# Kernel optimization log

Measured on AMD Instinct MI355X. Metric: run time of the kernel, lower is better.

Reference implementation:

```python
import jax, jax.numpy as jnp
import numpy as np

DIM = 128
N_NODES = 100000
N_EDGES = 600000
LN_EPS = 1e-5


def setup_inputs() -> dict:
    key = jax.random.key(0)
    k_x, k_ei, k_ew, k_w, k_b, k_g = jax.random.split(key, 6)
    x = jax.random.normal(k_x, (N_NODES, DIM), dtype=jnp.float32)
    edge_index = jax.random.randint(k_ei, (2, N_EDGES), 0, N_NODES, dtype=jnp.int64)
    edge_weight = jax.random.uniform(k_ew, (N_EDGES,), dtype=jnp.float32, minval=0.05, maxval=1.0)
    # GCNConv linear weight (glorot) + bias; LayerNorm affine params
    limit = float(np.sqrt(6.0 / (DIM + DIM)))
    W = jax.random.uniform(k_w, (DIM, DIM), dtype=jnp.float32, minval=-limit, maxval=limit)
    b = jnp.zeros((DIM,), dtype=jnp.float32)
    gamma = jnp.ones((DIM,), dtype=jnp.float32)
    beta = jnp.zeros((DIM,), dtype=jnp.float32)
    return {"x": x, "edge_index": edge_index, "edge_weight": edge_weight,
            "W": W, "b": b, "gamma": gamma, "beta": beta}


def reference(x, edge_index, edge_weight, W, b, gamma, beta):
    N = x.shape[0]
    row, col = edge_index[0], edge_index[1]  # messages flow row -> col (source_to_target)

    # gcn_norm (add_self_loops=False): deg[j] = sum of incoming edge weights
    deg = jax.ops.segment_sum(edge_weight, col, num_segments=N)
    deg_safe = jnp.where(deg > 0, deg, 1.0)
    dinv = jnp.where(deg > 0, jax.lax.rsqrt(deg_safe), 0.0)
    norm = dinv[row] * edge_weight * dinv[col]  # [E]

    h = x @ W                                   # [N, D] linear transform
    msg = h[row] * norm[:, None]                # gather + scale [E, D]
    agg = jax.ops.segment_sum(msg, col, num_segments=N) + b  # scatter-add [N, D]

    # LayerNorm over feature dim
    mu = jnp.mean(agg, axis=-1, keepdims=True)
    var = jnp.mean((agg - mu) ** 2, axis=-1, keepdims=True)
    ln = (agg - mu) * jax.lax.rsqrt(var + LN_EPS) * gamma + beta

    # GELU (torch default = exact erf form); dropout is identity at eval
    return x + jax.nn.gelu(ln, approximate=False)
```

## Files before the change

kernel.cpp:

```cpp
#include <hip/hip_runtime.h>
#include <hip/hip_fp16.h>
#include <math.h>

#define DIM 128
#define TR 32
#define SA_STRIDE 136
#define CSR_CAP 1024

#define DEG_SHIFT 42
#define DEG_SCALE 33554432.0f
#define DEG_MASK ((1ull << DEG_SHIFT) - 1)

typedef __attribute__((ext_vector_type(8))) short s16x8;
typedef __attribute__((ext_vector_type(4))) float f32x4;

__device__ __forceinline__ ushort f2bf(float f) {
    union { float f; unsigned u; } v; v.f = f;
    unsigned u = v.u;
    return (ushort)((u + 0x7FFFu + ((u >> 16) & 1u)) >> 16);
}

__device__ __forceinline__ ushort f2h(float f) {
    __half h = __float2half_rn(f);
    return *reinterpret_cast<ushort*>(&h);
}

__device__ __forceinline__ float h2f(ushort u) {
    __half_raw hr; hr.x = u;
    return __half2float(__half(hr));
}

__global__ void fill_zero(float* p, int n) {
    int i = blockIdx.x * blockDim.x + threadIdx.x;
    if (i < n) p[i] = 0.f;
}

__global__ void fill_zero4(float4* p, int n4) {
    int i = blockIdx.x * blockDim.x + threadIdx.x;
    if (i < n4) p[i] = make_float4(0.f, 0.f, 0.f, 0.f);
}

__global__ void init_kernel(const float* __restrict__ W, ushort* __restrict__ Wt,
                            float* __restrict__ zbase, int nz, int* __restrict__ gctr) {
    int i = blockIdx.x * blockDim.x + threadIdx.x;
    if (i < 16384) {
        int k = i >> 7, n = i & 127;
        Wt[n * DIM + k] = f2bf(W[k * DIM + n]);
    }
    int z = i - 16384;
    if (z >= 0 && z < nz) zbase[z] = 0.f;
    if (i == 0) *gctr = 0;
}

__global__ void count_deg_kernel(const int* __restrict__ ei, const float* __restrict__ ew,
                                 unsigned long long* __restrict__ cd,
                                 int* __restrict__ rank,
                                 const float* __restrict__ x, ushort* __restrict__ xh,
                                 int nxh, int E) {
    int e = blockIdx.x * blockDim.x + threadIdx.x;
    int nthreads = gridDim.x * blockDim.x;
    unsigned long long old = 0;
    bool valid = (e < E);
    if (valid) {
        int col = ei[E + e];
        unsigned long long pk = (1ull << DEG_SHIFT)
                              + (unsigned long long)(ew[e] * DEG_SCALE + 0.5f);
        old = atomicAdd(&cd[col], pk);
    }
    const float4* xs = (const float4*)x;
    for (int i = e; i < nxh; i += nthreads) {
        float4 a = xs[i * 2], c = xs[i * 2 + 1];
        s16x8 h;
        h[0] = (short)f2h(a.x); h[1] = (short)f2h(a.y);
        h[2] = (short)f2h(a.z); h[3] = (short)f2h(a.w);
        h[4] = (short)f2h(c.x); h[5] = (short)f2h(c.y);
        h[6] = (short)f2h(c.z); h[7] = (short)f2h(c.w);
        *(s16x8*)&xh[i * 8] = h;
    }
    if (valid) rank[e] = (int)(old >> DEG_SHIFT);
}

__global__ __launch_bounds__(256) void alloc_kernel(const unsigned long long* __restrict__ cd,
                                                    float* __restrict__ dinv,
                                                    int* __restrict__ row_start,
                                                    int* __restrict__ row_end,
                                                    int* __restrict__ gctr, int N) {
    __shared__ int wsum[4];
    __shared__ int sbase;
    int t = threadIdx.x;
    int i = blockIdx.x * 256 + t;
    int lane = t & 63;
    int w = t >> 6;
    unsigned long long p = (i < N) ? cd[i] : 0ull;
    int c = (int)(p >> DEG_SHIFT);
    int pre = c;
#pragma unroll
    for (int off = 1; off < 64; off <<= 1) {
        int v = __shfl_up(pre, off);
        if (lane >= off) pre += v;
    }
    if (lane == 63) wsum[w] = pre;
    __syncthreads();
    if (t == 0) sbase = atomicAdd(gctr, wsum[0] + wsum[1] + wsum[2] + wsum[3]);
    __syncthreads();
    int woff = 0;
#pragma unroll
    for (int k = 0; k < 3; ++k) if (w > k) woff += wsum[k];
    if (i < N) {
        int rs = sbase + woff + pre - c;
        row_start[i] = rs;
        row_end[i] = rs + c;
        float d = (float)(p & DEG_MASK) * (1.0f / DEG_SCALE);
        dinv[i] = d > 0.f ? rsqrtf(d) : 0.f;
    }
}

__global__ void csr_fill_kernel(const int* __restrict__ ei, const float* __restrict__ ew,
                                const int* __restrict__ rank,
                                const int* __restrict__ row_start,
                                const float* __restrict__ dinv,
                                int2* __restrict__ csr, int E) {
    int e = blockIdx.x * blockDim.x + threadIdx.x;
    if (e < E) {
        int row = ei[e];
        int col = ei[E + e];
        int p = row_start[col] + rank[e];
        float w = dinv[row] * ew[e];
        csr[p] = make_int2(row, __float_as_int(w));
    }
}

template<bool XH>
__global__ __launch_bounds__(256) void gather_mfma_ln_kernel(
        const int2* __restrict__ csr, const int* __restrict__ row_start,
        const int* __restrict__ seg_end, const float* __restrict__ dinv,
        const float* __restrict__ x, const ushort* __restrict__ xh,
        const ushort* __restrict__ Wt, const float* __restrict__ b,
        const float* __restrict__ gamma, const float* __restrict__ beta,
        float* __restrict__ out, int N) {
    __shared__ ushort sA[TR * SA_STRIDE];
    __shared__ int2 sCsr[CSR_CAP];
    __shared__ float redS[4][16];
    __shared__ float redQ[4][16];

    const int tid  = threadIdx.x;
    const int lane = tid & 63;
    const int w    = tid >> 6;
    const int row0 = blockIdx.x * TR;

    if (XH) {
        int lastNode = row0 + TR - 1; if (lastNode > N - 1) lastNode = N - 1;
        const int S = row_start[row0];
        const int T = seg_end[lastNode];
        const int M = T - S;
        const bool useLds = (M <= CSR_CAP);
        if (useLds) {
            for (int i = tid; i < M; i += 256) sCsr[i] = csr[S + i];
        }
        __syncthreads();

        const int l16 = tid & 15;
        const int g16 = tid >> 4;
        const s16x8* xh8 = (const s16x8*)xh;
        int sidx[2], eidx[2];
        float dv[2];
        float accq[2][8];
#pragma unroll
        for (int q = 0; q < 2; ++q) {
            int node = row0 + g16 * 2 + q;
            int ok = node < N;
            sidx[q] = ok ? row_start[node] : 0;
            eidx[q] = ok ? seg_end[node] : 0;
            dv[q]   = ok ? dinv[node] : 0.f;
#pragma unroll
            for (int e8 = 0; e8 < 8; ++e8) accq[q][e8] = 0.f;
        }

        if (useLds) {
#pragma unroll
            for (int q = 0; q < 2; ++q) {
                int sL = sidx[q] - S, eL = eidx[q] - S;
#pragma unroll 2
                for (int j = sL; j < eL; j += 2) {
                    int2 e0 = sCsr[j];
                    bool v1 = (j + 1) < eL;
                    int2 e1 = sCsr[v1 ? j + 1 : j];
                    float w0 = __int_as_float(e0.y);
                    float w1 = v1 ? __int_as_float(e1.y) : 0.f;
                    s16x8 r0 = xh8[(size_t)e0.x * 16 + l16];
                    s16x8 r1 = xh8[(size_t)e1.x * 16 + l16];
#pragma unroll
                    for (int e8 = 0; e8 < 8; ++e8) {
                        accq[q][e8] += w0 * h2f((ushort)r0[e8]);
                        accq[q][e8] += w1 * h2f((ushort)r1[e8]);
                    }
                }
            }
        } else {
            int maxlen = 0;
#pragma unroll
            for (int q = 0; q < 2; ++q) {
                int len = eidx[q] - sidx[q];
                maxlen = len > maxlen ? len : maxlen;
            }
#pragma unroll 2
            for (int it = 0; it < maxlen; ++it) {
                int2 pk[2];
#pragma unroll
                for (int q = 0; q < 2; ++q) {
                    int j = sidx[q] + it;
                    pk[q] = csr[j < eidx[q] ? j : 0];
                }
#pragma unroll
                for (int q = 0; q < 2; ++q) {
                    float wt = (sidx[q] + it < eidx[q]) ? __int_as_float(pk[q].y) : 0.f;
                    s16x8 hv = xh8[(size_t)pk[q].x * 16 + l16];
#pragma unroll
                    for (int e8 = 0; e8 < 8; ++e8)
                        accq[q][e8] += wt * h2f((ushort)hv[e8]);
                }
            }
        }
#pragma unroll
        for (int q = 0; q < 2; ++q) {
            int r = g16 * 2 + q;
            s16x8 p8;
#pragma unroll
            for (int e8 = 0; e8 < 8; ++e8) p8[e8] = (short)f2bf(accq[q][e8] * dv[q]);
            *(s16x8*)&sA[r * SA_STRIDE + l16 * 8] = p8;
        }
    } else {
        const int l32 = tid & 31;
        const int g32 = tid >> 5;
        const float4* xv = (const float4*)x;
        int sidx[4], eidx[4];
        float dv[4];
        float4 accq[4];
        int maxlen = 0;
#pragma unroll
        for (int q = 0; q < 4; ++q) {
            int node = row0 + g32 * 4 + q;
            int ok = node < N;
            sidx[q] = ok ? row_start[node] : 0;
            eidx[q] = ok ? seg_end[node] : 0;
            dv[q]   = ok ? dinv[node] : 0.f;
            accq[q] = make_float4(0.f, 0.f, 0.f, 0.f);
            int len = eidx[q] - sidx[q];
            maxlen = len > maxlen ? len : maxlen;
        }
#pragma unroll 2
        for (int it = 0; it < maxlen; ++it) {
            int2 pk[4];
#pragma unroll
            for (int q = 0; q < 4; ++q) {
                int j = sidx[q] + it;
                pk[q] = csr[j < eidx[q] ? j : 0];
            }
#pragma unroll
            for (int q = 0; q < 4; ++q) {
                float wt = (sidx[q] + it < eidx[q]) ? __int_as_float(pk[q].y) : 0.f;
                float4 v = xv[(size_t)pk[q].x * 32 + l32];
                accq[q].x += wt * v.x; accq[q].y += wt * v.y;
                accq[q].z += wt * v.z; accq[q].w += wt * v.w;
            }
        }
#pragma unroll
        for (int q = 0; q < 4; ++q) {
            int r = g32 * 4 + q;
            ushort4 p4;
            p4.x = f2bf(accq[q].x * dv[q]); p4.y = f2bf(accq[q].y * dv[q]);
            p4.z = f2bf(accq[q].z * dv[q]); p4.w = f2bf(accq[q].w * dv[q]);
            *(ushort4*)&sA[r * SA_STRIDE + l32 * 4] = p4;
        }
    }
    __syncthreads();

    const int m16  = lane & 15;
    const int quad = lane >> 4;
    const int tm   = w & 1;
    const int tnb  = (w >> 1) * 4;

    s16x8 afrag[4];
    const ushort* arow = &sA[(16 * tm + m16) * SA_STRIDE + quad * 8];
#pragma unroll
    for (int kb = 0; kb < 4; ++kb)
        afrag[kb] = *(const s16x8*)(arow + kb * 32);

    f32x4 acc[4];
#pragma unroll
    for (int t = 0; t < 4; ++t) { acc[t][0] = 0.f; acc[t][1] = 0.f; acc[t][2] = 0.f; acc[t][3] = 0.f; }

#pragma unroll
    for (int kb = 0; kb < 4; ++kb) {
#pragma unroll
        for (int t = 0; t < 4; ++t) {
            const ushort* bp = Wt + (size_t)((tnb + t) * 16 + m16) * DIM + kb * 32 + quad * 8;
            s16x8 bfrag = *(const s16x8*)bp;
            acc[t] = __builtin_amdgcn_mfma_f32_16x16x32_bf16(afrag[kb], bfrag, acc[t], 0, 0, 0);
        }
    }

    float gcol[4], becol[4];
#pragma unroll
    for (int t = 0; t < 4; ++t) {
        int col = (tnb + t) * 16 + m16;
        float bc = b[col];
        gcol[t]  = gamma[col];
        becol[t] = beta[col];
#pragma unroll
        for (int i = 0; i < 4; ++i) acc[t][i] += bc;
    }

    float s[4], sq[4];
#pragma unroll
    for (int i = 0; i < 4; ++i) {
        s[i]  = acc[0][i] + acc[1][i] + acc[2][i] + acc[3][i];
        sq[i] = acc[0][i]*acc[0][i] + acc[1][i]*acc[1][i] + acc[2][i]*acc[2][i] + acc[3][i]*acc[3][i];
    }
#pragma unroll
    for (int off = 1; off <= 8; off <<= 1) {
#pragma unroll
        for (int i = 0; i < 4; ++i) {
            s[i]  += __shfl_xor(s[i], off);
            sq[i] += __shfl_xor(sq[i], off);
        }
    }
    if (m16 == 0) {
#pragma unroll
        for (int i = 0; i < 4; ++i) {
            redS[w][quad * 4 + i] = s[i];
            redQ[w][quad * 4 + i] = sq[i];
        }
    }
    __syncthreads();

#pragma unroll
    for (int i = 0; i < 4; ++i) {
        int rloc = quad * 4 + i;
        float tot  = redS[w][rloc] + redS[w ^ 2][rloc];
        float totq = redQ[w][rloc] + redQ[w ^ 2][rloc];
        float mu   = tot * (1.0f / DIM);
        float var  = totq * (1.0f / DIM) - mu * mu;
        float rstd = rsqrtf(var + 1e-5f);
        int r = row0 + 16 * tm + rloc;
        if (r < N) {
#pragma unroll
            for (int t = 0; t < 4; ++t) {
                int col = (tnb + t) * 16 + m16;
                float l = (acc[t][i] - mu) * rstd * gcol[t] + becol[t];
                float g = 0.5f * l * (1.0f + erff(l * 0.70710678118654752f));
                out[(size_t)r * DIM + col] = x[(size_t)r * DIM + col] + g;
            }
        }
    }
}

__global__ void deg_kernel(const int* __restrict__ ei, const float* __restrict__ ew,
                           float* __restrict__ deg, int E) {
    int e = blockIdx.x * blockDim.x + threadIdx.x;
    if (e < E) atomicAdd(&deg[ei[E + e]], ew[e]);
}

__global__ void dinv_kernel(float* deg, int N) {
    int i = blockIdx.x * blockDim.x + threadIdx.x;
    if (i < N) {
        float d = deg[i];
        deg[i] = d > 0.f ? rsqrtf(d) : 0.f;
    }
}

__global__ void scatter_kernel(const int* __restrict__ ei, const float* __restrict__ ew,
                               const float* __restrict__ dinv, const float* __restrict__ x,
                               float* __restrict__ out, int E) {
    int t = blockIdx.x * blockDim.x + threadIdx.x;
    int e = t >> 5;
    if (e >= E) return;
    int lane = t & 31;
    int row = ei[e];
    int col = ei[E + e];
    float w = dinv[row] * ew[e] * dinv[col];
    float4 v = *(const float4*)(x + (size_t)row * DIM + (lane << 2));
    float* dst = out + (size_t)col * DIM + (lane << 2);
    atomicAdd(dst + 0, v.x * w);
    atomicAdd(dst + 1, v.y * w);
    atomicAdd(dst + 2, v.z * w);
    atomicAdd(dst + 3, v.w * w);
}

__global__ __launch_bounds__(256) void gemm_ln_kernel(const float* __restrict__ x,
                                                      const float* __restrict__ W,
                                                      const float* __restrict__ b,
                                                      const float* __restrict__ gamma,
                                                      const float* __restrict__ beta,
                                                      float* __restrict__ out, int N) {
    __shared__ float sT[DIM][TR + 4];
    const int tid = threadIdx.x;
    const int row0 = blockIdx.x * TR;
    {
        int r = tid >> 3;
        int c0 = (tid & 7) << 4;
        int rr = row0 + r; if (rr > N - 1) rr = N - 1;
        const float4* src = (const float4*)(out + (size_t)rr * DIM + c0);
#pragma unroll
        for (int i = 0; i < 4; ++i) {
            float4 v = src[i];
            int c = c0 + i * 4;
            sT[c + 0][r] = v.x; sT[c + 1][r] = v.y; sT[c + 2][r] = v.z; sT[c + 3][r] = v.w;
        }
    }
    __syncthreads();
    const int tx = tid & 31;
    const int ty = tid >> 5;
    float acc[4][4] = {};
    const float4* Wv = (const float4*)W;
#pragma unroll 4
    for (int k = 0; k < DIM; ++k) {
        float4 wv = Wv[k * 32 + tx];
        float4 a  = *(const float4*)(&sT[k][ty * 4]);
        acc[0][0] += a.x * wv.x; acc[0][1] += a.x * wv.y; acc[0][2] += a.x * wv.z; acc[0][3] += a.x * wv.w;
        acc[1][0] += a.y * wv.x; acc[1][1] += a.y * wv.y; acc[1][2] += a.y * wv.z; acc[1][3] += a.y * wv.w;
        acc[2][0] += a.z * wv.x; acc[2][1] += a.z * wv.y; acc[2][2] += a.z * wv.z; acc[2][3] += a.z * wv.w;
        acc[3][0] += a.w * wv.x; acc[3][1] += a.w * wv.y; acc[3][2] += a.w * wv.z; acc[3][3] += a.w * wv.w;
    }
    float4 b4 = ((const float4*)b)[tx];
#pragma unroll
    for (int i = 0; i < 4; ++i) {
        acc[i][0] += b4.x; acc[i][1] += b4.y; acc[i][2] += b4.z; acc[i][3] += b4.w;
    }
    float4 g4  = ((const float4*)gamma)[tx];
    float4 be4 = ((const float4*)beta)[tx];
#pragma unroll
    for (int i = 0; i < 4; ++i) {
        float s  = acc[i][0] + acc[i][1] + acc[i][2] + acc[i][3];
        float sq = acc[i][0]*acc[i][0] + acc[i][1]*acc[i][1] + acc[i][2]*acc[i][2] + acc[i][3]*acc[i][3];
#pragma unroll
        for (int off = 16; off > 0; off >>= 1) {
            s  += __shfl_xor(s, off);
            sq += __shfl_xor(sq, off);
        }
        float mu   = s * (1.0f / DIM);
        float var  = sq * (1.0f / DIM) - mu * mu;
        float rstd = rsqrtf(var + 1e-5f);
        int r = row0 + ty * 4 + i;
        if (r < N) {
            float4 xr = *(const float4*)(x + (size_t)r * DIM + tx * 4);
            float lg[4] = {g4.x, g4.y, g4.z, g4.w};
            float lb[4] = {be4.x, be4.y, be4.z, be4.w};
            float lx[4] = {xr.x, xr.y, xr.z, xr.w};
            float o[4];
#pragma unroll
            for (int c = 0; c < 4; ++c) {
                float l = (acc[i][c] - mu) * rstd * lg[c] + lb[c];
                float g = 0.5f * l * (1.0f + erff(l * 0.70710678118654752f));
                o[c] = lx[c] + g;
            }
            *(float4*)(out + (size_t)r * DIM + tx * 4) = make_float4(o[0], o[1], o[2], o[3]);
        }
    }
}

extern "C" void kernel_launch(void* const* d_in, const int* in_sizes, int n_in,
                              void* d_out, int out_size, void* d_ws, size_t ws_size,
                              hipStream_t stream) {
    const float* x     = (const float*)d_in[0];
    const int*   ei    = (const int*)d_in[1];
    const float* ew    = (const float*)d_in[2];
    const float* W     = (const float*)d_in[3];
    const float* b     = (const float*)d_in[4];
    const float* gamma = (const float*)d_in[5];
    const float* beta  = (const float*)d_in[6];
    const int N = in_sizes[0] / DIM;
    const int E = in_sizes[2];
    float* out = (float*)d_out;

    const int nb = (N + 255) / 256;

    size_t hdr_words = 8192 + (size_t)5 * N + (size_t)E + 1;
    hdr_words = (hdr_words + 3) & ~(size_t)3;
    size_t xh_words = (size_t)N * (DIM / 2);
    size_t need_basic = (hdr_words + (size_t)2 * E) * sizeof(float);
    size_t need_xh    = (hdr_words + xh_words + (size_t)2 * E) * sizeof(float);

    if (ws_size >= need_basic) {
        const bool use_xh = (ws_size >= need_xh);
        ushort* Wt         = (ushort*)d_ws;
        unsigned long long* cd = (unsigned long long*)((float*)d_ws + 8192);
        float*  dinv       = (float*)d_ws + 8192 + (size_t)2 * N;
        int*    row_start  = (int*)(dinv + N);
        int*    row_end    = row_start + N;
        int*    rank       = row_end + N;
        int*    gctr       = rank + E;
        ushort* xh         = (ushort*)((float*)d_ws + hdr_words);
        int2*   csr        = (int2*)((float*)d_ws + hdr_words + (use_xh ? xh_words : 0));

        int nxh = use_xh ? N * (DIM / 8) : 0;
        int initn = 16384 + 2 * N;
        init_kernel<<<(initn + 255) / 256, 256, 0, stream>>>(W, Wt, (float*)cd, 2 * N, gctr);
        count_deg_kernel<<<(E + 255) / 256, 256, 0, stream>>>(ei, ew, cd, rank, x, xh, nxh, E);
        alloc_kernel<<<nb, 256, 0, stream>>>(cd, dinv, row_start, row_end, gctr, N);
        csr_fill_kernel<<<(E + 255) / 256, 256, 0, stream>>>(ei, ew, rank, row_start, dinv, csr, E);

        if (use_xh) {
            gather_mfma_ln_kernel<true><<<(N + TR - 1) / TR, 256, 0, stream>>>(
                csr, row_start, row_end, dinv, x, xh, Wt, b, gamma, beta, out, N);
        } else {
            gather_mfma_ln_kernel<false><<<(N + TR - 1) / TR, 256, 0, stream>>>(
                csr, row_start, row_end, dinv, x, xh, Wt, b, gamma, beta, out, N);
        }
    } else {
        float* deg = (float*)d_ws;
        int n4 = N * DIM / 4;
        fill_zero4<<<(n4 + 255) / 256, 256, 0, stream>>>((float4*)out, n4);
        fill_zero<<<nb, 256, 0, stream>>>(deg, N);
        deg_kernel<<<(E + 255) / 256, 256, 0, stream>>>(ei, ew, deg, E);
        dinv_kernel<<<nb, 256, 0, stream>>>(deg, N);
        long long sthreads = (long long)E * 32;
        scatter_kernel<<<(int)((sthreads + 255) / 256), 256, 0, stream>>>(ei, ew, deg, x, out, E);
        gemm_ln_kernel<<<(N + TR - 1) / TR, 256, 0, stream>>>(x, W, b, gamma, beta, out, N);
    }
}
```

Before: 226.2 us.

## Shard degree-count atomics across 8 per-block-group copies with 32-bit packing

Packs the edge count and fixed-point degree into one 32-bit word instead of a 64-bit one, and splits the counter array into 8 shards chosen by block index so that concurrent atomics to the same column are spread out. The allocation kernel sums the shards, computes per-shard base offsets for the CSR layout, and the fill kernel uses the shard base plus rank. The aim is to cut atomic contention and 64-bit atomic cost. In exchange, init has more zeroing work, extra shard reads and writes, and the fixed-point degree has less precision (2^20 scale, 26-bit field).

```diff
diff --git a/kernel.cpp b/kernel.cpp
--- a/kernel.cpp
+++ b/kernel.cpp
@@ -7,9 +7,9 @@
 #define SA_STRIDE 136
 #define CSR_CAP 1024
 
-#define DEG_SHIFT 42
-#define DEG_SCALE 33554432.0f
-#define DEG_MASK ((1ull << DEG_SHIFT) - 1)
+#define CNT_SHIFT 26
+#define DEGW_SCALE 1048576.0f
+#define DEGW_MASK ((1u << CNT_SHIFT) - 1)
 
 typedef __attribute__((ext_vector_type(8))) short s16x8;
 typedef __attribute__((ext_vector_type(4))) float f32x4;
@@ -53,19 +53,18 @@
 }
 
 __global__ void count_deg_kernel(const int* __restrict__ ei, const float* __restrict__ ew,
-                                 unsigned long long* __restrict__ cd,
-                                 int* __restrict__ rank,
+                                 unsigned* __restrict__ cd, int* __restrict__ rank,
                                  const float* __restrict__ x, ushort* __restrict__ xh,
-                                 int nxh, int E) {
+                                 int nxh, int E, int N, int shardMask) {
     int e = blockIdx.x * blockDim.x + threadIdx.x;
     int nthreads = gridDim.x * blockDim.x;
-    unsigned long long old = 0;
+    unsigned old = 0;
     bool valid = (e < E);
     if (valid) {
         int col = ei[E + e];
-        unsigned long long pk = (1ull << DEG_SHIFT)
-                              + (unsigned long long)(ew[e] * DEG_SCALE + 0.5f);
-        old = atomicAdd(&cd[col], pk);
+        unsigned pk = (1u << CNT_SHIFT) + (unsigned)(ew[e] * DEGW_SCALE + 0.5f);
+        int shard = blockIdx.x & shardMask;
+        old = atomicAdd(&cd[(size_t)shard * N + col], pk);
     }
     const float4* xs = (const float4*)x;
     for (int i = e; i < nxh; i += nthreads) {
@@ -77,23 +76,35 @@
         h[6] = (short)f2h(c.z); h[7] = (short)f2h(c.w);
         *(s16x8*)&xh[i * 8] = h;
     }
-    if (valid) rank[e] = (int)(old >> DEG_SHIFT);
-}
-
-__global__ __launch_bounds__(256) void alloc_kernel(const unsigned long long* __restrict__ cd,
+    if (valid) rank[e] = (int)(old >> CNT_SHIFT);
+}
+
+__global__ __launch_bounds__(256) void alloc_kernel(const unsigned* __restrict__ cd,
                                                     float* __restrict__ dinv,
                                                     int* __restrict__ row_start,
                                                     int* __restrict__ row_end,
-                                                    int* __restrict__ gctr, int N) {
+                                                    int* __restrict__ sbase,
+                                                    int* __restrict__ gctr, int N, int nshard) {
     __shared__ int wsum[4];
-    __shared__ int sbase;
+    __shared__ int sb;
     int t = threadIdx.x;
     int i = blockIdx.x * 256 + t;
     int lane = t & 63;
     int w = t >> 6;
-    unsigned long long p = (i < N) ? cd[i] : 0ull;
-    int c = (int)(p >> DEG_SHIFT);
-    int pre = c;
+    int cnt_s[8];
+    int cnt = 0;
+    unsigned degfx = 0;
+#pragma unroll 8
+    for (int s = 0; s < 8; ++s) cnt_s[s] = 0;
+    if (i < N) {
+        for (int s = 0; s < nshard; ++s) {
+            unsigned v = cd[(size_t)s * N + i];
+            cnt_s[s] = (int)(v >> CNT_SHIFT);
+            degfx += v & DEGW_MASK;
+            cnt += cnt_s[s];
+        }
+    }
+    int pre = cnt;
 #pragma unroll
     for (int off = 1; off < 64; off <<= 1) {
         int v = __shfl_up(pre, off);
@@ -101,30 +112,36 @@
     }
     if (lane == 63) wsum[w] = pre;
     __syncthreads();
-    if (t == 0) sbase = atomicAdd(gctr, wsum[0] + wsum[1] + wsum[2] + wsum[3]);
+    if (t == 0) sb = atomicAdd(gctr, wsum[0] + wsum[1] + wsum[2] + wsum[3]);
     __syncthreads();
     int woff = 0;
 #pragma unroll
     for (int k = 0; k < 3; ++k) if (w > k) woff += wsum[k];
     if (i < N) {
-        int rs = sbase + woff + pre - c;
+        int rs = sb + woff + pre - cnt;
         row_start[i] = rs;
-        row_end[i] = rs + c;
-        float d = (float)(p & DEG_MASK) * (1.0f / DEG_SCALE);
+        row_end[i] = rs + cnt;
+        int off = rs;
+        for (int s = 0; s < nshard; ++s) {
+            sbase[(size_t)s * N + i] = off;
+            off += cnt_s[s];
+        }
+        float d = (float)degfx * (1.0f / DEGW_SCALE);
         dinv[i] = d > 0.f ? rsqrtf(d) : 0.f;
     }
 }
 
 __global__ void csr_fill_kernel(const int* __restrict__ ei, const float* __restrict__ ew,
                                 const int* __restrict__ rank,
-                                const int* __restrict__ row_start,
+                                const int* __restrict__ sbase,
                                 const float* __restrict__ dinv,
-                                int2* __restrict__ csr, int E) {
+                                int2* __restrict__ csr, int E, int N, int shardMask) {
     int e = blockIdx.x * blockDim.x + threadIdx.x;
     if (e < E) {
         int row = ei[e];
         int col = ei[E + e];
-        int p = row_start[col] + rank[e];
+        int shard = (e >> 8) & shardMask;
+        int p = sbase[(size_t)shard * N + col] + rank[e];
         float w = dinv[row] * ew[e];
         csr[p] = make_int2(row, __float_as_int(w));
     }
@@ -475,30 +492,43 @@
 
     const int nb = (N + 255) / 256;
 
-    size_t hdr_words = 8192 + (size_t)5 * N + (size_t)E + 1;
-    hdr_words = (hdr_words + 3) & ~(size_t)3;
     size_t xh_words = (size_t)N * (DIM / 2);
-    size_t need_basic = (hdr_words + (size_t)2 * E) * sizeof(float);
-    size_t need_xh    = (hdr_words + xh_words + (size_t)2 * E) * sizeof(float);
-
-    if (ws_size >= need_basic) {
-        const bool use_xh = (ws_size >= need_xh);
-        ushort* Wt         = (ushort*)d_ws;
-        unsigned long long* cd = (unsigned long long*)((float*)d_ws + 8192);
-        float*  dinv       = (float*)d_ws + 8192 + (size_t)2 * N;
-        int*    row_start  = (int*)(dinv + N);
-        int*    row_end    = row_start + N;
-        int*    rank       = row_end + N;
-        int*    gctr       = rank + E;
-        ushort* xh         = (ushort*)((float*)d_ws + hdr_words);
-        int2*   csr        = (int2*)((float*)d_ws + hdr_words + (use_xh ? xh_words : 0));
-
+    auto hdrw = [&](int ns) {
+        size_t h = 8192 + (size_t)(2 * ns + 3) * N + (size_t)E + 1;
+        return (h + 3) & ~(size_t)3;
+    };
+    size_t need8  = (hdrw(8) + xh_words + (size_t)2 * E) * sizeof(float);
+    size_t need1x = (hdrw(1) + xh_words + (size_t)2 * E) * sizeof(float);
+    size_t need1  = (hdrw(1) + (size_t)2 * E) * sizeof(float);
+
+    int nshard = 0;
+    bool use_xh = false;
+    if (ws_size >= need8)       { nshard = 8; use_xh = true;  }
+    else if (ws_size >= need1x) { nshard = 1; use_xh = true;  }
+    else if (ws_size >= need1)  { nshard = 1; use_xh = false; }
+
+    if (nshard > 0) {
+        size_t hdr = hdrw(nshard);
+        ushort*   Wt        = (ushort*)d_ws;
+        unsigned* cd        = (unsigned*)((float*)d_ws + 8192);
+        float*    dinv      = (float*)d_ws + 8192 + (size_t)nshard * N;
+        int*      row_start = (int*)(dinv + N);
+        int*      row_end   = row_start + N;
+        int*      sbase     = row_end + N;
+        int*      rank      = sbase + (size_t)nshard * N;
+        int*      gctr      = rank + E;
+        ushort*   xh        = (ushort*)((float*)d_ws + hdr);
+        int2*     csr       = (int2*)((float*)d_ws + hdr + (use_xh ? xh_words : 0));
+
+        int nz = nshard * N;
         int nxh = use_xh ? N * (DIM / 8) : 0;
-        int initn = 16384 + 2 * N;
-        init_kernel<<<(initn + 255) / 256, 256, 0, stream>>>(W, Wt, (float*)cd, 2 * N, gctr);
-        count_deg_kernel<<<(E + 255) / 256, 256, 0, stream>>>(ei, ew, cd, rank, x, xh, nxh, E);
-        alloc_kernel<<<nb, 256, 0, stream>>>(cd, dinv, row_start, row_end, gctr, N);
-        csr_fill_kernel<<<(E + 255) / 256, 256, 0, stream>>>(ei, ew, rank, row_start, dinv, csr, E);
+        int initn = 16384 + nz;
+        init_kernel<<<(initn + 255) / 256, 256, 0, stream>>>(W, Wt, (float*)cd, nz, gctr);
+        count_deg_kernel<<<(E + 255) / 256, 256, 0, stream>>>(
+            ei, ew, cd, rank, x, xh, nxh, E, N, nshard - 1);
+        alloc_kernel<<<nb, 256, 0, stream>>>(cd, dinv, row_start, row_end, sbase, gctr, N, nshard);
+        csr_fill_kernel<<<(E + 255) / 256, 256, 0, stream>>>(
+            ei, ew, rank, sbase, dinv, csr, E, N, nshard - 1);
 
         if (use_xh) {
             gather_mfma_ln_kernel<true><<<(N + TR - 1) / TR, 256, 0, stream>>>(
```

After: 227.8 us. About the same (+0.7%).

## Fuse CSR preprocessing into one cooperative kernel and unroll gather by three

Applied to the files above, without the earlier changes.

Merges the four preprocessing launches (weight transpose, degree count, prefix allocation, CSR fill) into a single cooperative kernel that uses grid-wide syncs between phases, with the original launches kept as a fallback if the cooperative launch fails. This targets per-launch overhead and idle gaps between small kernels. The LDS gather loop also processes three edges per iteration instead of two to expose more loads in flight. The cooperative grid is fixed at 1024 blocks, so the grid syncs and fixed occupancy may cost more than the launch overhead they replace.

```diff
diff --git a/kernel.cpp b/kernel.cpp
--- a/kernel.cpp
+++ b/kernel.cpp
@@ -1,6 +1,9 @@
 #include <hip/hip_runtime.h>
 #include <hip/hip_fp16.h>
+#include <hip/hip_cooperative_groups.h>
 #include <math.h>
+
+namespace cg = cooperative_groups;
 
 #define DIM 128
 #define TR 32
@@ -38,6 +41,88 @@
 __global__ void fill_zero4(float4* p, int n4) {
     int i = blockIdx.x * blockDim.x + threadIdx.x;
     if (i < n4) p[i] = make_float4(0.f, 0.f, 0.f, 0.f);
+}
+
+__global__ __launch_bounds__(256) void preproc_coop(
+        const float* __restrict__ W, ushort* __restrict__ Wt,
+        const float* __restrict__ x, ushort* __restrict__ xh, int nxh,
+        const int* __restrict__ ei, const float* __restrict__ ew,
+        unsigned long long* __restrict__ cd, int* __restrict__ rank,
+        float* __restrict__ dinv, int* __restrict__ row_start,
+        int* __restrict__ row_end, int* __restrict__ gctr,
+        int2* __restrict__ csr, int N, int E, int nchunks) {
+    cg::grid_group grid = cg::this_grid();
+    const int tid  = blockIdx.x * blockDim.x + threadIdx.x;
+    const int nthr = gridDim.x * blockDim.x;
+
+    for (int i = tid; i < 16384; i += nthr) {
+        int k = i >> 7, n = i & 127;
+        Wt[n * DIM + k] = f2bf(W[k * DIM + n]);
+    }
+    int* cdz = (int*)cd;
+    for (int i = tid; i < 2 * N; i += nthr) cdz[i] = 0;
+    if (tid == 0) *gctr = 0;
+    const float4* xs = (const float4*)x;
+    for (int i = tid; i < nxh; i += nthr) {
+        float4 a = xs[i * 2], c = xs[i * 2 + 1];
+        s16x8 h;
+        h[0] = (short)f2h(a.x); h[1] = (short)f2h(a.y);
+        h[2] = (short)f2h(a.z); h[3] = (short)f2h(a.w);
+        h[4] = (short)f2h(c.x); h[5] = (short)f2h(c.y);
+        h[6] = (short)f2h(c.z); h[7] = (short)f2h(c.w);
+        *(s16x8*)&xh[i * 8] = h;
+    }
+    grid.sync();
+
+    for (int e = tid; e < E; e += nthr) {
+        int col = ei[E + e];
+        unsigned long long pk = (1ull << DEG_SHIFT)
+                              + (unsigned long long)(ew[e] * DEG_SCALE + 0.5f);
+        unsigned long long old = atomicAdd(&cd[col], pk);
+        rank[e] = (int)(old >> DEG_SHIFT);
+    }
+    grid.sync();
+
+    __shared__ int wsum[4];
+    __shared__ int sb;
+    for (int chunk = blockIdx.x; chunk < nchunks; chunk += gridDim.x) {
+        int t = threadIdx.x;
+        int i = chunk * 256 + t;
+        int lane = t & 63;
+        int w = t >> 6;
+        unsigned long long p = (i < N) ? cd[i] : 0ull;
+        int c = (int)(p >> DEG_SHIFT);
+        int pre = c;
+#pragma unroll
+        for (int off = 1; off < 64; off <<= 1) {
+            int v = __shfl_up(pre, off);
+            if (lane >= off) pre += v;
+        }
+        if (lane == 63) wsum[w] = pre;
+        __syncthreads();
+        if (t == 0) sb = atomicAdd(gctr, wsum[0] + wsum[1] + wsum[2] + wsum[3]);
+        __syncthreads();
+        int woff = 0;
+#pragma unroll
+        for (int k = 0; k < 3; ++k) if (w > k) woff += wsum[k];
+        if (i < N) {
+            int rs = sb + woff + pre - c;
+            row_start[i] = rs;
+            row_end[i] = rs + c;
+            float d = (float)(p & DEG_MASK) * (1.0f / DEG_SCALE);
+            dinv[i] = d > 0.f ? rsqrtf(d) : 0.f;
+        }
+        __syncthreads();
+    }
+    grid.sync();
+
+    for (int e = tid; e < E; e += nthr) {
+        int row = ei[e];
+        int col = ei[E + e];
+        int p = row_start[col] + rank[e];
+        float wv = dinv[row] * ew[e];
+        csr[p] = make_int2(row, __float_as_int(wv));
+    }
 }
 
 __global__ void init_kernel(const float* __restrict__ W, ushort* __restrict__ Wt,
@@ -86,7 +171,7 @@
                                                     int* __restrict__ row_end,
                                                     int* __restrict__ gctr, int N) {
     __shared__ int wsum[4];
-    __shared__ int sbase;
+    __shared__ int sb;
     int t = threadIdx.x;
     int i = blockIdx.x * 256 + t;
     int lane = t & 63;
@@ -101,13 +186,13 @@
     }
     if (lane == 63) wsum[w] = pre;
     __syncthreads();
-    if (t == 0) sbase = atomicAdd(gctr, wsum[0] + wsum[1] + wsum[2] + wsum[3]);
+    if (t == 0) sb = atomicAdd(gctr, wsum[0] + wsum[1] + wsum[2] + wsum[3]);
     __syncthreads();
     int woff = 0;
 #pragma unroll
     for (int k = 0; k < 3; ++k) if (w > k) woff += wsum[k];
     if (i < N) {
-        int rs = sbase + woff + pre - c;
+        int rs = sb + woff + pre - c;
         row_start[i] = rs;
         row_end[i] = rs + c;
         float d = (float)(p & DEG_MASK) * (1.0f / DEG_SCALE);
@@ -181,18 +266,23 @@
             for (int q = 0; q < 2; ++q) {
                 int sL = sidx[q] - S, eL = eidx[q] - S;
 #pragma unroll 2
-                for (int j = sL; j < eL; j += 2) {
+                for (int j = sL; j < eL; j += 3) {
                     int2 e0 = sCsr[j];
                     bool v1 = (j + 1) < eL;
+                    bool v2 = (j + 2) < eL;
                     int2 e1 = sCsr[v1 ? j + 1 : j];
+                    int2 e2 = sCsr[v2 ? j + 2 : j];
                     float w0 = __int_as_float(e0.y);
                     float w1 = v1 ? __int_as_float(e1.y) : 0.f;
+                    float w2 = v2 ? __int_as_float(e2.y) : 0.f;
                     s16x8 r0 = xh8[(size_t)e0.x * 16 + l16];
                     s16x8 r1 = xh8[(size_t)e1.x * 16 + l16];
+                    s16x8 r2 = xh8[(size_t)e2.x * 16 + l16];
 #pragma unroll
                     for (int e8 = 0; e8 < 8; ++e8) {
                         accq[q][e8] += w0 * h2f((ushort)r0[e8]);
                         accq[q][e8] += w1 * h2f((ushort)r1[e8]);
+                        accq[q][e8] += w2 * h2f((ushort)r2[e8]);
                     }
                 }
             }
@@ -494,11 +584,26 @@
         int2*   csr        = (int2*)((float*)d_ws + hdr_words + (use_xh ? xh_words : 0));
 
         int nxh = use_xh ? N * (DIM / 8) : 0;
-        int initn = 16384 + 2 * N;
-        init_kernel<<<(initn + 255) / 256, 256, 0, stream>>>(W, Wt, (float*)cd, 2 * N, gctr);
-        count_deg_kernel<<<(E + 255) / 256, 256, 0, stream>>>(ei, ew, cd, rank, x, xh, nxh, E);
-        alloc_kernel<<<nb, 256, 0, stream>>>(cd, dinv, row_start, row_end, gctr, N);
-        csr_fill_kernel<<<(E + 255) / 256, 256, 0, stream>>>(ei, ew, rank, row_start, dinv, csr, E);
+        int nchunks = nb;
+        int Nv = N, Ev = E;
+        const float* Wp = W; ushort* Wtp = Wt;
+        const float* xp = x; ushort* xhp = xh;
+        const int* eip = ei; const float* ewp = ew;
+        unsigned long long* cdp = cd; int* rankp = rank;
+        float* dinvp = dinv; int* rsp = row_start; int* rep = row_end;
+        int* gctrp = gctr; int2* csrp = csr;
+        void* kargs[] = { &Wp, &Wtp, &xp, &xhp, &nxh, &eip, &ewp, &cdp, &rankp,
+                          &dinvp, &rsp, &rep, &gctrp, &csrp, &Nv, &Ev, &nchunks };
+        hipError_t cerr = hipLaunchCooperativeKernel((void*)preproc_coop,
+                                                     dim3(1024), dim3(256),
+                                                     kargs, 0, stream);
+        if (cerr != hipSuccess) {
+            int initn = 16384 + 2 * N;
+            init_kernel<<<(initn + 255) / 256, 256, 0, stream>>>(W, Wt, (float*)cd, 2 * N, gctr);
+            count_deg_kernel<<<(E + 255) / 256, 256, 0, stream>>>(ei, ew, cd, rank, x, xh, nxh, E);
+            alloc_kernel<<<nb, 256, 0, stream>>>(cd, dinv, row_start, row_end, gctr, N);
+            csr_fill_kernel<<<(E + 255) / 256, 256, 0, stream>>>(ei, ew, rank, row_start, dinv, csr, E);
+        }
 
         if (use_xh) {
             gather_mfma_ln_kernel<true><<<(N + TR - 1) / TR, 256, 0, stream>>>(
```

After: 563.9 us. 149% more time.
